# Performance work log

Hardware: AMD Instinct MI355X
Metric: run time of the kernel (lower is better)

Reference implementation:

```python
import jax, jax.numpy as jnp
import numpy as np


def dht(x):
    # Discrete Hartley transform over spatial dims via FFT (ortho norm):
    # H(x) = Re(F(x)) - Im(F(x)). With norm='ortho' the DHT is its own inverse.
    X = jnp.fft.fftn(x, axes=(2, 3), norm='ortho')
    return X.real - X.imag


def _neg_freq(a):
    # H[-k] = roll(flip(H), 1) along both spectral dims
    return jnp.roll(jnp.flip(a, axis=(-2, -1)), shift=(1, 1), axis=(-2, -1))


def compl_mul2d(x1, x2):
    x1n = _neg_freq(x1)
    x2n = _neg_freq(x2)
    return 0.5 * (
        jnp.einsum('bixy,ioxy->boxy', x1, x2)
        - jnp.einsum('bixy,ioxy->boxy', x1n, x2n)
        + jnp.einsum('bixy,ioxy->boxy', x1, x2n)
        + jnp.einsum('bixy,ioxy->boxy', x1n, x2)
    )


def setup_inputs() -> dict:
    key = jax.random.key(0)
    k1, k2 = jax.random.split(key)
    B, Ci, Co, S, M = 16, 32, 32, 256, 16
    x = jax.random.normal(k1, (B, Ci, S, S), dtype=jnp.float32)
    scale = 1.0 / (Ci * Co)
    weights1 = scale * jax.random.uniform(k2, (Ci, Co, M, M), dtype=jnp.float32)
    return {'x': x, 'weights1': weights1}


def reference(x, weights1):
    B = x.shape[0]
    S1, S2 = x.shape[-2], x.shape[-1]
    Co = weights1.shape[1]
    m1, m2 = weights1.shape[2], weights1.shape[3]
    x_ht = dht(x)                                   # [B, Ci, S1, S2]
    res = compl_mul2d(x_ht[:, :, :m1, :m2], weights1)  # [B, Co, m1, m2]
    out_ht = jnp.zeros((B, Co, S1, S2), dtype=x.dtype).at[:, :, :m1, :m2].set(res)
    return dht(out_ht)                              # inverse DHT == DHT (ortho)
```

## Files before the change

kernel.cpp:

```cpp
#include <hip/hip_runtime.h>

#define CI 32
#define CO 32

constexpr float INV_S = 1.0f / 256.0f;
constexpr float THETA = 6.28318530717958647692f / 256.0f;

typedef float f32x16 __attribute__((ext_vector_type(16)));

__device__ __forceinline__ f32x16 sload16(const float* p) {
  f32x16 r;
  asm volatile("s_load_dwordx16 %0, %1, 0x0\n\ts_waitcnt lgkmcnt(0)"
               : "=&s"(r) : "s"(p));
  return r;
}

__device__ __forceinline__ void sload2x16_64(const float* p, f32x16& a, f32x16& b) {
  asm volatile("s_load_dwordx16 %0, %2, 0x0\n\t"
               "s_load_dwordx16 %1, %2, 0x40\n\t"
               "s_waitcnt lgkmcnt(0)"
               : "=&s"(a), "=&s"(b) : "s"(p));
}

__device__ __forceinline__ void sload2x16_16k(const float* p, f32x16& a, f32x16& b) {
  asm volatile("s_load_dwordx16 %0, %2, 0x0\n\t"
               "s_load_dwordx16 %1, %2, 0x4000\n\t"
               "s_waitcnt lgkmcnt(0)"
               : "=&s"(a), "=&s"(b) : "s"(p));
}

__global__ void k_tab(float* __restrict__ TCb, float* __restrict__ TSb,
                      float* __restrict__ TPb, float* __restrict__ TMb) {
  const int t = threadIdx.x;
  #pragma unroll
  for (int k = 0; k < 16; ++k) {
    float s, c;
    sincosf(THETA * (float)((k * t) & 255), &s, &c);
    TCb[t * 16 + k] = c;
    TSb[t * 16 + k] = s;
    TPb[k * 256 + t] = c + s;
    TMb[k * 256 + t] = c - s;
  }
}

__global__ __launch_bounds__(256, 2) void k_fwd(const float* __restrict__ x,
                                                const float* __restrict__ TCb,
                                                const float* __restrict__ TPb,
                                                const float* __restrict__ TMb,
                                                float* __restrict__ xh) {
  __shared__ __align__(16) float C1[16][260];
  __shared__ __align__(16) float S1[16][260];
  const int t = threadIdx.x;
  const float* __restrict__ xp = x + (size_t)blockIdx.x * 65536 + t;

  float aC[16], aS[16];
  {
    float x0 = xp[0];
    float xm = xp[128 * 256];
    float e = x0 + xm, o = x0 - xm;
    #pragma unroll
    for (int k = 0; k < 16; ++k) { aC[k] = (k & 1) ? o : e; aS[k] = 0.f; }
  }

  for (int base = 1; base + 8 <= 121; base += 8) {
    float xlo[8], xhi[8];
    #pragma unroll
    for (int j = 0; j < 8; ++j) {
      xlo[j] = xp[(base + j) * 256];
      xhi[j] = xp[(256 - base - j) * 256];
    }
    #pragma unroll
    for (int j = 0; j < 8; ++j) {
      const int n = base + j;
      f32x16 tc, ts;
      sload2x16_16k(TCb + n * 16, tc, ts);
      float es = xlo[j] + xhi[j];
      float ds = xlo[j] - xhi[j];
      #pragma unroll
      for (int k = 0; k < 16; ++k) {
        aC[k] = fmaf(es, tc[k], aC[k]);
        aS[k] = fmaf(ds, ts[k], aS[k]);
      }
    }
  }
  for (int n = 121; n < 128; ++n) {
    float lo = xp[n * 256];
    float hi = xp[(256 - n) * 256];
    f32x16 tc, ts;
    sload2x16_16k(TCb + n * 16, tc, ts);
    float es = lo + hi, ds = lo - hi;
    #pragma unroll
    for (int k = 0; k < 16; ++k) {
      aC[k] = fmaf(es, tc[k], aC[k]);
      aS[k] = fmaf(ds, ts[k], aS[k]);
    }
  }

  #pragma unroll
  for (int k = 0; k < 16; ++k) { C1[k][t] = aC[k]; S1[k][t] = aS[k]; }
  __syncthreads();

  const int k1 = t >> 4, k2 = t & 15;
  const float* __restrict__ tp = TPb + k2 * 256;
  const float* __restrict__ tm = TMb + k2 * 256;
  float acc = 0.f;
  #pragma unroll 2
  for (int n2 = 0; n2 < 256; n2 += 4) {
    const float4 c4 = *(const float4*)&C1[k1][n2];
    const float4 s4 = *(const float4*)&S1[k1][n2];
    const float4 p4 = *(const float4*)&tp[n2];
    const float4 m4 = *(const float4*)&tm[n2];
    acc = fmaf(c4.x, p4.x, acc); acc = fmaf(s4.x, m4.x, acc);
    acc = fmaf(c4.y, p4.y, acc); acc = fmaf(s4.y, m4.y, acc);
    acc = fmaf(c4.z, p4.z, acc); acc = fmaf(s4.z, m4.z, acc);
    acc = fmaf(c4.w, p4.w, acc); acc = fmaf(s4.w, m4.w, acc);
  }
  xh[(size_t)blockIdx.x * 256 + t] = acc * INV_S;
}

__global__ __launch_bounds__(256, 2) void k_mid(const float* __restrict__ xh,
                                                const float* __restrict__ w,
                                                float* __restrict__ Wout) {
  __shared__ float xs[CI][256];
  __shared__ __align__(16) float rsm[256];
  const int t = threadIdx.x;
  const int b = blockIdx.x >> 5;
  const int o = blockIdx.x & 31;

  #pragma unroll 8
  for (int i = 0; i < CI; ++i)
    xs[i][t] = xh[(size_t)(b * CI + i) * 256 + t];
  __syncthreads();

  const int k1 = t >> 4, k2 = t & 15;
  const int tn = (((16 - k1) & 15) << 4) | ((16 - k2) & 15);
  float acc = 0.f;
  #pragma unroll 8
  for (int i = 0; i < CI; ++i) {
    const float* __restrict__ wrow = w + (size_t)(i * CO + o) * 256;
    float wp = wrow[t];
    float wn = wrow[tn];
    float xv = xs[i][t];
    float xnv = xs[i][tn];
    acc = fmaf(xv, wp + wn, acc);
    acc = fmaf(xnv, wp - wn, acc);
  }
  rsm[t] = 0.5f * acc;
  __syncthreads();

  if (t <= 128) {
    float cc[16], ssn[16];
    #pragma unroll
    for (int k = 0; k < 16; ++k)
      sincosf(THETA * (float)((k * t) & 255), &ssn[k], &cc[k]);
    float U[16], V[16];
    #pragma unroll
    for (int j = 0; j < 16; ++j) { U[j] = 0.f; V[j] = 0.f; }
    #pragma unroll
    for (int kk1 = 0; kk1 < 16; ++kk1) {
      float c = cc[kk1], s = ssn[kk1];
      #pragma unroll
      for (int j = 0; j < 16; ++j) {
        float r = rsm[kk1 * 16 + j];
        U[j] = fmaf(c, r, U[j]);
        V[j] = fmaf(s, r, V[j]);
      }
    }
    float* __restrict__ wr = Wout + (size_t)blockIdx.x * 4128 + t * 32;
    #pragma unroll
    for (int j = 0; j < 16; ++j) {
      wr[j] = U[j] * INV_S;
      wr[16 + j] = V[j] * INV_S;
    }
  }
}

__global__ __launch_bounds__(256, 4) void k_invB(const float* __restrict__ Wb,
                                                 float* __restrict__ out) {
  const int t = threadIdx.x;
  const int img = blockIdx.x >> 1;
  const int half = blockIdx.x & 1;

  float cp[16], cm[16];
  #pragma unroll
  for (int k = 0; k < 16; ++k) {
    float s, c;
    sincosf(THETA * (float)((k * t) & 255), &s, &c);
    cp[k] = c + s;
    cm[k] = c - s;
  }

  const float* __restrict__ wbase = Wb + (size_t)img * 4128;
  float* __restrict__ op = out + (size_t)img * 65536 + t;

  const int n_lo = half ? 65 : 0;
  const int n_hi = half ? 128 : 64;
  for (int n = n_lo; n <= n_hi; ++n) {
    f32x16 uu, vv;
    sload2x16_64(wbase + n * 32, uu, vv);
    float a = 0.f, bsum = 0.f;
    #pragma unroll
    for (int k = 0; k < 16; ++k) {
      a = fmaf(uu[k], cp[k], a);
      bsum = fmaf(vv[k], cm[k], bsum);
    }
    op[(size_t)n * 256] = a + bsum;
    if (n >= 1 && n <= 127) op[(size_t)(256 - n) * 256] = a - bsum;
  }
}

extern "C" void kernel_launch(void* const* d_in, const int* in_sizes, int n_in,
                              void* d_out, int out_size, void* d_ws, size_t ws_size,
                              hipStream_t stream) {
  const float* x = (const float*)d_in[0];
  const float* w = (const float*)d_in[1];
  float* out = (float*)d_out;

  float* TCb = (float*)d_ws;
  float* TSb = TCb + 4096;
  float* TPb = TSb + 4096;
  float* TMb = TPb + 4096;
  float* xh  = TMb + 4096;
  float* Wb  = xh + 131072;

  k_tab<<<1, 256, 0, stream>>>(TCb, TSb, TPb, TMb);
  k_fwd<<<16 * CI, 256, 0, stream>>>(x, TCb, TPb, TMb, xh);
  k_mid<<<16 * CO, 256, 0, stream>>>(xh, w, Wb);
  k_invB<<<2 * 16 * CO, 256, 0, stream>>>(Wb, out);
}
```

Baseline: 308.5 us.

## Replace twiddle tables with on-the-fly rotation recurrences and drop table kernel

Removes the k_tab launch and the precomputed twiddle tables. k_fwd now generates twiddles through complex rotation recurrences, with periodic sincos resyncs, and software-prefetches the next batch of input rows. The mid kernel spreads its inverse row transform across all 256 threads with vectorized stores and a padded Wout stride, and k_invB swaps scalar s_load reads for float4 vector loads. This saves one launch plus the table traffic at the cost of extra FMAs per step and some accumulated rounding error from the recurrences.

```diff
diff --git a/kernel.cpp b/kernel.cpp
--- a/kernel.cpp
+++ b/kernel.cpp
@@ -6,47 +6,18 @@
 constexpr float INV_S = 1.0f / 256.0f;
 constexpr float THETA = 6.28318530717958647692f / 256.0f;
 
-typedef float f32x16 __attribute__((ext_vector_type(16)));
-
-__device__ __forceinline__ f32x16 sload16(const float* p) {
-  f32x16 r;
-  asm volatile("s_load_dwordx16 %0, %1, 0x0\n\ts_waitcnt lgkmcnt(0)"
-               : "=&s"(r) : "s"(p));
-  return r;
-}
-
-__device__ __forceinline__ void sload2x16_64(const float* p, f32x16& a, f32x16& b) {
-  asm volatile("s_load_dwordx16 %0, %2, 0x0\n\t"
-               "s_load_dwordx16 %1, %2, 0x40\n\t"
-               "s_waitcnt lgkmcnt(0)"
-               : "=&s"(a), "=&s"(b) : "s"(p));
-}
-
-__device__ __forceinline__ void sload2x16_16k(const float* p, f32x16& a, f32x16& b) {
-  asm volatile("s_load_dwordx16 %0, %2, 0x0\n\t"
-               "s_load_dwordx16 %1, %2, 0x4000\n\t"
-               "s_waitcnt lgkmcnt(0)"
-               : "=&s"(a), "=&s"(b) : "s"(p));
-}
-
-__global__ void k_tab(float* __restrict__ TCb, float* __restrict__ TSb,
-                      float* __restrict__ TPb, float* __restrict__ TMb) {
-  const int t = threadIdx.x;
-  #pragma unroll
-  for (int k = 0; k < 16; ++k) {
-    float s, c;
-    sincosf(THETA * (float)((k * t) & 255), &s, &c);
-    TCb[t * 16 + k] = c;
-    TSb[t * 16 + k] = s;
-    TPb[k * 256 + t] = c + s;
-    TMb[k * 256 + t] = c - s;
-  }
-}
+__device__ constexpr float RC[16] = {
+  1.0f,          0.9996988187f, 0.9987954562f, 0.9972904567f,
+  0.9951847267f, 0.9924795346f, 0.9891765100f, 0.9852776424f,
+  0.9807852804f, 0.9757021300f, 0.9700312532f, 0.9637760658f,
+  0.9569403357f, 0.9495281806f, 0.9415440652f, 0.9329927988f};
+__device__ constexpr float RS[16] = {
+  0.0f,          0.0245412285f, 0.0490676743f, 0.0735645636f,
+  0.0980171403f, 0.1224106752f, 0.1467304745f, 0.1709618888f,
+  0.1950903220f, 0.2191012402f, 0.2429801799f, 0.2667127575f,
+  0.2902846773f, 0.3136817404f, 0.3368898534f, 0.3598950365f};
 
 __global__ __launch_bounds__(256, 2) void k_fwd(const float* __restrict__ x,
-                                                const float* __restrict__ TCb,
-                                                const float* __restrict__ TPb,
-                                                const float* __restrict__ TMb,
                                                 float* __restrict__ xh) {
   __shared__ __align__(16) float C1[16][260];
   __shared__ __align__(16) float S1[16][260];
@@ -62,37 +33,64 @@
     for (int k = 0; k < 16; ++k) { aC[k] = (k & 1) ? o : e; aS[k] = 0.f; }
   }
 
-  for (int base = 1; base + 8 <= 121; base += 8) {
-    float xlo[8], xhi[8];
+  float tc[16], ts[16];
+  #pragma unroll
+  for (int k = 0; k < 16; ++k) { tc[k] = RC[k]; ts[k] = RS[k]; }
+
+  float xl[8], xhb[8], nxl[8], nxh[8];
+  #pragma unroll
+  for (int j = 0; j < 8; ++j) {
+    xl[j] = xp[(1 + j) * 256];
+    xhb[j] = xp[(255 - j) * 256];
+  }
+
+  int n0 = 1;
+  for (int c = 0; c < 15; ++c, n0 += 8) {
+    if (c == 4 || c == 8 || c == 12) {
+      #pragma unroll
+      for (int k = 0; k < 16; ++k)
+        sincosf(THETA * (float)((n0 * k) & 255), &ts[k], &tc[k]);
+    }
+    if (c < 14) {
+      #pragma unroll
+      for (int j = 0; j < 8; ++j) {
+        nxl[j] = xp[(n0 + 8 + j) * 256];
+        nxh[j] = xp[(248 - n0 - j) * 256];
+      }
+    } else {
+      #pragma unroll
+      for (int j = 0; j < 7; ++j) {
+        nxl[j] = xp[(121 + j) * 256];
+        nxh[j] = xp[(135 - j) * 256];
+      }
+    }
     #pragma unroll
     for (int j = 0; j < 8; ++j) {
-      xlo[j] = xp[(base + j) * 256];
-      xhi[j] = xp[(256 - base - j) * 256];
-    }
-    #pragma unroll
-    for (int j = 0; j < 8; ++j) {
-      const int n = base + j;
-      f32x16 tc, ts;
-      sload2x16_16k(TCb + n * 16, tc, ts);
-      float es = xlo[j] + xhi[j];
-      float ds = xlo[j] - xhi[j];
+      float es = xl[j] + xhb[j];
+      float ds = xl[j] - xhb[j];
       #pragma unroll
       for (int k = 0; k < 16; ++k) {
         aC[k] = fmaf(es, tc[k], aC[k]);
         aS[k] = fmaf(ds, ts[k], aS[k]);
-      }
-    }
-  }
-  for (int n = 121; n < 128; ++n) {
-    float lo = xp[n * 256];
-    float hi = xp[(256 - n) * 256];
-    f32x16 tc, ts;
-    sload2x16_16k(TCb + n * 16, tc, ts);
-    float es = lo + hi, ds = lo - hi;
+        float nc = fmaf(-ts[k], RS[k], tc[k] * RC[k]);
+        float ns = fmaf(tc[k], RS[k], ts[k] * RC[k]);
+        tc[k] = nc; ts[k] = ns;
+      }
+    }
+    #pragma unroll
+    for (int j = 0; j < 8; ++j) { xl[j] = nxl[j]; xhb[j] = nxh[j]; }
+  }
+  #pragma unroll
+  for (int j = 0; j < 7; ++j) {
+    float es = xl[j] + xhb[j];
+    float ds = xl[j] - xhb[j];
     #pragma unroll
     for (int k = 0; k < 16; ++k) {
       aC[k] = fmaf(es, tc[k], aC[k]);
       aS[k] = fmaf(ds, ts[k], aS[k]);
+      float nc = fmaf(-ts[k], RS[k], tc[k] * RC[k]);
+      float ns = fmaf(tc[k], RS[k], ts[k] * RC[k]);
+      tc[k] = nc; ts[k] = ns;
     }
   }
 
@@ -101,19 +99,28 @@
   __syncthreads();
 
   const int k1 = t >> 4, k2 = t & 15;
-  const float* __restrict__ tp = TPb + k2 * 256;
-  const float* __restrict__ tm = TMb + k2 * 256;
+  float rc2, rs2;
+  sincosf(THETA * (float)k2, &rs2, &rc2);
   float acc = 0.f;
-  #pragma unroll 2
-  for (int n2 = 0; n2 < 256; n2 += 4) {
-    const float4 c4 = *(const float4*)&C1[k1][n2];
-    const float4 s4 = *(const float4*)&S1[k1][n2];
-    const float4 p4 = *(const float4*)&tp[n2];
-    const float4 m4 = *(const float4*)&tm[n2];
-    acc = fmaf(c4.x, p4.x, acc); acc = fmaf(s4.x, m4.x, acc);
-    acc = fmaf(c4.y, p4.y, acc); acc = fmaf(s4.y, m4.y, acc);
-    acc = fmaf(c4.z, p4.z, acc); acc = fmaf(s4.z, m4.z, acc);
-    acc = fmaf(c4.w, p4.w, acc); acc = fmaf(s4.w, m4.w, acc);
+  #pragma unroll
+  for (int q = 0; q < 4; ++q) {
+    const int m = (q * k2) & 3;
+    float cc = (m == 0) ? 1.f : (m == 2) ? -1.f : 0.f;
+    float ss = (m == 1) ? 1.f : (m == 3) ? -1.f : 0.f;
+    #pragma unroll 2
+    for (int n2 = q * 64; n2 < q * 64 + 64; n2 += 4) {
+      float c4[4], s4[4];
+      *(float4*)c4 = *(const float4*)&C1[k1][n2];
+      *(float4*)s4 = *(const float4*)&S1[k1][n2];
+      #pragma unroll
+      for (int jj = 0; jj < 4; ++jj) {
+        acc = fmaf(c4[jj], cc + ss, acc);
+        acc = fmaf(s4[jj], cc - ss, acc);
+        float nc = fmaf(-ss, rs2, cc * rc2);
+        float ns = fmaf(cc, rs2, ss * rc2);
+        cc = nc; ss = ns;
+      }
+    }
   }
   xh[(size_t)blockIdx.x * 256 + t] = acc * INV_S;
 }
@@ -140,38 +147,60 @@
     const float* __restrict__ wrow = w + (size_t)(i * CO + o) * 256;
     float wp = wrow[t];
     float wn = wrow[tn];
-    float xv = xs[i][t];
-    float xnv = xs[i][tn];
-    acc = fmaf(xv, wp + wn, acc);
-    acc = fmaf(xnv, wp - wn, acc);
+    acc = fmaf(xs[i][t], wp + wn, acc);
+    acc = fmaf(xs[i][tn], wp - wn, acc);
   }
   rsm[t] = 0.5f * acc;
   __syncthreads();
 
-  if (t <= 128) {
-    float cc[16], ssn[16];
-    #pragma unroll
-    for (int k = 0; k < 16; ++k)
-      sincosf(THETA * (float)((k * t) & 255), &ssn[k], &cc[k]);
-    float U[16], V[16];
-    #pragma unroll
-    for (int j = 0; j < 16; ++j) { U[j] = 0.f; V[j] = 0.f; }
-    #pragma unroll
-    for (int kk1 = 0; kk1 < 16; ++kk1) {
-      float c = cc[kk1], s = ssn[kk1];
-      #pragma unroll
-      for (int j = 0; j < 16; ++j) {
-        float r = rsm[kk1 * 16 + j];
-        U[j] = fmaf(c, r, U[j]);
-        V[j] = fmaf(s, r, V[j]);
-      }
-    }
-    float* __restrict__ wr = Wout + (size_t)blockIdx.x * 4128 + t * 32;
-    #pragma unroll
-    for (int j = 0; j < 16; ++j) {
-      wr[j] = U[j] * INV_S;
-      wr[16 + j] = V[j] * INV_S;
-    }
+  const int row = t & 127, h = t >> 7;
+  float cc[16], ss[16];
+  #pragma unroll
+  for (int k = 0; k < 16; ++k)
+    sincosf(THETA * (float)((k * row) & 255), &ss[k], &cc[k]);
+  float U[8], V[8];
+  #pragma unroll
+  for (int j = 0; j < 8; ++j) { U[j] = 0.f; V[j] = 0.f; }
+  #pragma unroll
+  for (int k = 0; k < 16; ++k) {
+    float ra[8];
+    *(float4*)&ra[0] = *(const float4*)&rsm[k * 16 + 8 * h];
+    *(float4*)&ra[4] = *(const float4*)&rsm[k * 16 + 8 * h + 4];
+    #pragma unroll
+    for (int j = 0; j < 8; ++j) {
+      U[j] = fmaf(cc[k], ra[j], U[j]);
+      V[j] = fmaf(ss[k], ra[j], V[j]);
+    }
+  }
+  float* __restrict__ wr = Wout + (size_t)blockIdx.x * 4160 + row * 32 + 8 * h;
+  {
+    float4 u0 = {U[0]*INV_S, U[1]*INV_S, U[2]*INV_S, U[3]*INV_S};
+    float4 u1 = {U[4]*INV_S, U[5]*INV_S, U[6]*INV_S, U[7]*INV_S};
+    float4 v0 = {V[0]*INV_S, V[1]*INV_S, V[2]*INV_S, V[3]*INV_S};
+    float4 v1 = {V[4]*INV_S, V[5]*INV_S, V[6]*INV_S, V[7]*INV_S};
+    *(float4*)&wr[0] = u0; *(float4*)&wr[4] = u1;
+    *(float4*)&wr[16] = v0; *(float4*)&wr[20] = v1;
+  }
+
+  if (row == 0) {
+    float U8[8];
+    #pragma unroll
+    for (int j = 0; j < 8; ++j) U8[j] = 0.f;
+    #pragma unroll
+    for (int k = 0; k < 16; ++k) {
+      float ra[8];
+      *(float4*)&ra[0] = *(const float4*)&rsm[k * 16 + 8 * h];
+      *(float4*)&ra[4] = *(const float4*)&rsm[k * 16 + 8 * h + 4];
+      #pragma unroll
+      for (int j = 0; j < 8; ++j)
+        U8[j] = (k & 1) ? (U8[j] - ra[j]) : (U8[j] + ra[j]);
+    }
+    float* __restrict__ wr8 = Wout + (size_t)blockIdx.x * 4160 + 128 * 32 + 8 * h;
+    float4 a0 = {U8[0]*INV_S, U8[1]*INV_S, U8[2]*INV_S, U8[3]*INV_S};
+    float4 a1 = {U8[4]*INV_S, U8[5]*INV_S, U8[6]*INV_S, U8[7]*INV_S};
+    float4 z = {0.f, 0.f, 0.f, 0.f};
+    *(float4*)&wr8[0] = a0; *(float4*)&wr8[4] = a1;
+    *(float4*)&wr8[16] = z; *(float4*)&wr8[20] = z;
   }
 }
 
@@ -190,14 +219,19 @@
     cm[k] = c - s;
   }
 
-  const float* __restrict__ wbase = Wb + (size_t)img * 4128;
+  const float* __restrict__ wbase = Wb + (size_t)img * 4160;
   float* __restrict__ op = out + (size_t)img * 65536 + t;
 
   const int n_lo = half ? 65 : 0;
   const int n_hi = half ? 128 : 64;
+  #pragma unroll 2
   for (int n = n_lo; n <= n_hi; ++n) {
-    f32x16 uu, vv;
-    sload2x16_64(wbase + n * 32, uu, vv);
+    float uu[16], vv[16];
+    #pragma unroll
+    for (int q = 0; q < 4; ++q) {
+      *(float4*)&uu[4 * q] = *(const float4*)(wbase + n * 32 + 4 * q);
+      *(float4*)&vv[4 * q] = *(const float4*)(wbase + n * 32 + 16 + 4 * q);
+    }
     float a = 0.f, bsum = 0.f;
     #pragma unroll
     for (int k = 0; k < 16; ++k) {
@@ -216,15 +250,10 @@
   const float* w = (const float*)d_in[1];
   float* out = (float*)d_out;
 
-  float* TCb = (float*)d_ws;
-  float* TSb = TCb + 4096;
-  float* TPb = TSb + 4096;
-  float* TMb = TPb + 4096;
-  float* xh  = TMb + 4096;
-  float* Wb  = xh + 131072;
-
-  k_tab<<<1, 256, 0, stream>>>(TCb, TSb, TPb, TMb);
-  k_fwd<<<16 * CI, 256, 0, stream>>>(x, TCb, TPb, TMb, xh);
-  k_mid<<<16 * CO, 256, 0, stream>>>(xh, w, Wb);
+  float* xhb = (float*)d_ws;
+  float* Wb  = xhb + 131072;
+
+  k_fwd<<<16 * CI, 256, 0, stream>>>(x, xhb);
+  k_mid<<<16 * CO, 256, 0, stream>>>(xhb, w, Wb);
   k_invB<<<2 * 16 * CO, 256, 0, stream>>>(Wb, out);
 }
```

Measured after the change: 277.8 us. 1.11x faster.
